# Performance work log

Measured on AMD Instinct MI355X. Metric: run time of the kernel, lower is better.

The kernel has to match this reference:

```python
import jax, jax.numpy as jnp
import numpy as np

NUM_CLASSES = 81
NEG_POS_RATIO = 3  # neg_pos init arg
POS_FRAC = 0.02    # realistic fraction of matched (positive) priors


def setup_inputs() -> dict:
    key = jax.random.key(0)
    k1, k2, k3, k4, k5 = jax.random.split(key, 5)
    B, P, C = 32, 24564, NUM_CLASSES
    loc_data = jax.random.normal(k1, (B, P, 4), jnp.float32)
    conf_data = jax.random.normal(k2, (B, P, C), jnp.float32)
    loc_targets = jax.random.normal(k3, (B, P, 4), jnp.float32)
    raw_labels = jax.random.randint(k4, (B, P), 1, C)
    is_pos = jax.random.uniform(k5, (B, P)) < POS_FRAC
    conf_targets = jnp.where(is_pos, raw_labels, 0).astype(jnp.int32)
    return {"loc_data": loc_data, "conf_data": conf_data,
            "loc_targets": loc_targets, "conf_targets": conf_targets}


def _smooth_l1(x):
    ax = jnp.abs(x)
    return jnp.where(ax < 1.0, 0.5 * x * x, ax - 0.5)


def reference(loc_data, conf_data, loc_targets, conf_targets):
    # loc_data [B,P,4], conf_data [B,P,C], conf_targets [B,P] int
    B, P, C = conf_data.shape
    pos = conf_targets > 0  # [B,P]

    # localization smooth-L1 over positive priors only (sum reduction)
    loc_loss = jnp.sum(_smooth_l1(loc_data - loc_targets) * pos[..., None].astype(loc_data.dtype))

    # per-prior CE loss: logsumexp - logit[target]
    lse = jax.nn.logsumexp(conf_data, axis=-1)  # [B,P]
    tgt_logit = jnp.take_along_axis(conf_data, conf_targets[..., None].astype(jnp.int32), axis=-1)[..., 0]
    ce = lse - tgt_logit  # [B,P]

    # hard negative mining: zero out positives, sort descending, pick pivot at 3*num_pos
    mined = jnp.where(pos, 0.0, ce)
    sorted_desc = jnp.flip(jnp.sort(mined, axis=1), axis=1)  # [B,P]
    num_pos = jnp.sum(pos, axis=1)  # [B]
    num_neg = jnp.clip(NEG_POS_RATIO * num_pos, 0, P - 1)
    pivot = jnp.take_along_axis(sorted_desc, num_neg[:, None], axis=1)  # [B,1]
    neg = mined > pivot

    sel = (pos | neg).astype(ce.dtype)
    conf_loss = jnp.sum(ce * sel)

    n_matched = jnp.maximum(jnp.sum(num_pos), 1).astype(conf_data.dtype)
    return (loc_loss + conf_loss) / n_matched
```

## Files before the change

### kernel.cpp

```cpp
#include <hip/hip_runtime.h>
#include <cmath>
#include <cstdint>

#define NB 32
#define NP 24564
#define NC 81
#define NEG_POS 3

static constexpr size_t MINED_ELEMS = (size_t)NB * NP;
static constexpr size_t MINED_BYTES = MINED_ELEMS * sizeof(float);

#define NTILES4 ((int)(MINED_ELEMS / 4))
#define MAIN_BLOCKS 2047
#define TOTAL_WAVES (MAIN_BLOCKS * 4)
#define KITERS 12


__device__ __forceinline__ float wave_reduce_sum(float v) {
#pragma unroll
  for (int off = 32; off > 0; off >>= 1) v += __shfl_down(v, off, 64);
  return v;
}

__device__ __forceinline__ float smooth_l1_4(float4 a, float4 t) {
  float acc = 0.f, d, ax;
  d = a.x - t.x; ax = fabsf(d); acc += (ax < 1.f) ? 0.5f * d * d : ax - 0.5f;
  d = a.y - t.y; ax = fabsf(d); acc += (ax < 1.f) ? 0.5f * d * d : ax - 0.5f;
  d = a.z - t.z; ax = fabsf(d); acc += (ax < 1.f) ? 0.5f * d * d : ax - 0.5f;
  d = a.w - t.w; ax = fabsf(d); acc += (ax < 1.f) ? 0.5f * d * d : ax - 0.5f;
  return acc;
}

__global__ __launch_bounds__(256, 8) void mb_main(
    const float* __restrict__ conf_data, const int* __restrict__ conf_targets,
    float* __restrict__ mined) {
  __shared__ float lds[4][332];

  const int tid  = (int)threadIdx.x;
  const int wid  = tid >> 6, lane = tid & 63;
  const int r    = lane >> 4, il = lane & 15;
  float* __restrict__ L = lds[wid];

  const int l17   = (lane < 17) ? lane : 16;
  const int ldst1 = (lane < 17) ? (256 + 4 * l17) : 328;

#define LOAD_DATA(c0, c1, t)                                            \
  do {                                                                  \
    const float4* __restrict__ _s =                                     \
        reinterpret_cast<const float4*>(conf_data) + (size_t)(t) * 81;  \
    (c0) = _s[lane];                                                    \
    (c1) = _s[64 + l17];                                                \
  } while (0)

#define STAGE(c0, c1)                                  \
  do {                                                 \
    *reinterpret_cast<float4*>(&L[4 * lane]) = (c0);   \
    *reinterpret_cast<float4*>(&L[ldst1]) = (c1);      \
  } while (0)

#define COMPUTE(t, tg)                                                  \
  do {                                                                  \
    const int tgt = (r == 0) ? (tg).x : (r == 1) ? (tg).y               \
                  : (r == 2) ? (tg).z : (tg).w;                         \
    const int rb = 81 * r;                                              \
    float e = __expf(L[rb + il]) + __expf(L[rb + il + 16]) +            \
              __expf(L[rb + il + 32]) + __expf(L[rb + il + 48]) +       \
              __expf(L[rb + il + 64]);                                  \
    if (il == 0) e += __expf(L[rb + 80]);                               \
    e += __shfl_xor(e, 1, 64);                                          \
    e += __shfl_xor(e, 2, 64);                                          \
    e += __shfl_xor(e, 4, 64);                                          \
    e += __shfl_xor(e, 8, 64);                                          \
    const float tv = L[rb + tgt];                                       \
    const float ce = __logf(e) - tv;                                    \
    const float val = (tgt > 0) ? -ce : ce;                             \
    mined[(t) * 4 + r] = val;                                           \
  } while (0)

  int tile = (int)blockIdx.x * 4 + wid;
  float4 cA0, cA1, cB0, cB1;
  int4 tg0, tg1, tgN;

  LOAD_DATA(cA0, cA1, tile);
  tg0 = *reinterpret_cast<const int4*>(conf_targets + (size_t)tile * 4);
  {
    const int tB = tile + TOTAL_WAVES;
    LOAD_DATA(cB0, cB1, tB);
    tg1 = *reinterpret_cast<const int4*>(conf_targets + (size_t)tB * 4);
  }

#pragma unroll 1
  for (int k = 0; k < KITERS; ++k) {
    STAGE(cA0, cA1);
    {
      int nt = tile + 2 * TOTAL_WAVES;
      nt = (nt < NTILES4) ? nt : tile;
      LOAD_DATA(cA0, cA1, nt);
      tgN = *reinterpret_cast<const int4*>(conf_targets + (size_t)nt * 4);
    }
    __builtin_amdgcn_sched_barrier(0);
    COMPUTE(tile, tg0);
    tg0 = tg1; tg1 = tgN;
    tile += TOTAL_WAVES;

    STAGE(cB0, cB1);
    {
      int nt = tile + 2 * TOTAL_WAVES;
      nt = (nt < NTILES4) ? nt : tile;
      LOAD_DATA(cB0, cB1, nt);
      tgN = *reinterpret_cast<const int4*>(conf_targets + (size_t)nt * 4);
    }
    __builtin_amdgcn_sched_barrier(0);
    COMPUTE(tile, tg0);
    tg0 = tg1; tg1 = tgN;
    tile += TOTAL_WAVES;
  }
#undef LOAD_DATA
#undef STAGE
#undef COMPUTE
}

__global__ __launch_bounds__(1024) void mb_select(
    const float* __restrict__ mined, const float* __restrict__ loc_data,
    const float* __restrict__ loc_targets, float* __restrict__ partial,
    int* __restrict__ num_pos) {
  const int b = blockIdx.x;
  const float* __restrict__ row = mined + (size_t)b * NP;
  const int tid = threadIdx.x;
  const int wid = tid >> 6;
  const int lane = tid & 63;

  __shared__ int hist[16][256];
  __shared__ int total[256];
  __shared__ int suffix[256];
  __shared__ unsigned s_prefix;
  __shared__ int s_k;

  for (int i = tid; i < 16 * 256; i += 1024) ((int*)hist)[i] = 0;
  __syncthreads();
  {
    int np = 0;
    float cp = 0.f, lv = 0.f;
    for (int q = tid; q < NP / 4; q += 1024) {
      const float4 v = reinterpret_cast<const float4*>(row)[q];
      const float vv[4] = {v.x, v.y, v.z, v.w};
#pragma unroll
      for (int j = 0; j < 4; ++j) {
        unsigned u = __float_as_uint(vv[j]);
        if (u >> 31) {
          np++;
          cp += -vv[j];
          const size_t flat = (size_t)b * NP + 4 * q + j;
          lv += smooth_l1_4(
              *reinterpret_cast<const float4*>(loc_data + flat * 4),
              *reinterpret_cast<const float4*>(loc_targets + flat * 4));
          u = 0u;
        }
        atomicAdd(&hist[wid][u >> 24], 1);
      }
    }
    __shared__ float rednp[16], redcp[16], redlv[16];
    float wnp = wave_reduce_sum((float)np);
    float wcp = wave_reduce_sum(cp);
    float wlv = wave_reduce_sum(lv);
    if (lane == 0) { rednp[wid] = wnp; redcp[wid] = wcp; redlv[wid] = wlv; }
    __syncthreads();
    if (tid == 0) {
      float tnp = 0.f, tcp = 0.f, tlv = 0.f;
#pragma unroll
      for (int i = 0; i < 16; ++i) { tnp += rednp[i]; tcp += redcp[i]; tlv += redlv[i]; }
      const int npi = (int)tnp;
      num_pos[b] = npi;
      partial[b * 4 + 0] = tlv;
      partial[b * 4 + 1] = tcp;
      int k = NEG_POS * npi;
      if (k > NP - 1) k = NP - 1;
      s_k = k;
      s_prefix = 0u;
    }
    __syncthreads();
  }

#define PASS_EPILOGUE(SHIFT)                                                  \
  do {                                                                        \
    if (tid < 256) {                                                          \
      int t = 0;                                                              \
      _Pragma("unroll")                                                       \
      for (int w = 0; w < 16; ++w) t += hist[w][tid];                         \
      total[tid] = t;                                                         \
    }                                                                         \
    __syncthreads();                                                          \
    if (wid == 0) {                                                           \
      const int t0_ = total[4 * lane + 0];                                    \
      const int t1_ = total[4 * lane + 1];                                    \
      const int t2_ = total[4 * lane + 2];                                    \
      const int t3_ = total[4 * lane + 3];                                    \
      const int s3 = t3_;                                                     \
      const int s2 = t2_ + s3;                                                \
      const int s1 = t1_ + s2;                                                \
      const int s0 = t0_ + s1;                                                \
      int acc_ = s0;                                                          \
      _Pragma("unroll")                                                       \
      for (int off = 1; off < 64; off <<= 1) {                                \
        const int o = __shfl_down(acc_, off, 64);                             \
        if (lane + off < 64) acc_ += o;                                       \
      }                                                                       \
      const int excl = acc_ - s0;                                             \
      suffix[4 * lane + 0] = s0 + excl;                                       \
      suffix[4 * lane + 1] = s1 + excl;                                       \
      suffix[4 * lane + 2] = s2 + excl;                                       \
      suffix[4 * lane + 3] = s3 + excl;                                       \
    }                                                                         \
    __syncthreads();                                                          \
    if (tid < 256) {                                                          \
      const int kcur = s_k;                                                   \
      const int cs = suffix[tid] - total[tid];                                \
      if (kcur >= cs && kcur < cs + total[tid]) {                             \
        s_prefix |= ((unsigned)tid << (SHIFT));                               \
        s_k = kcur - cs;                                                      \
      }                                                                       \
    }                                                                         \
    __syncthreads();                                                          \
  } while (0)

  PASS_EPILOGUE(24);

  for (int shift = 16; shift >= 0; shift -= 8) {
    for (int i = tid; i < 16 * 256; i += 1024) ((int*)hist)[i] = 0;
    __syncthreads();
    const unsigned mask = 0xFFFFFFFFu << (shift + 8);
    const unsigned pfx = s_prefix;

    for (int q = tid; q < NP / 4; q += 1024) {
      const float4 v = reinterpret_cast<const float4*>(row)[q];
      unsigned u;
      u = __float_as_uint(v.x); u = (u >> 31) ? 0u : u; if ((u & mask) == pfx) atomicAdd(&hist[wid][(u >> shift) & 255], 1);
      u = __float_as_uint(v.y); u = (u >> 31) ? 0u : u; if ((u & mask) == pfx) atomicAdd(&hist[wid][(u >> shift) & 255], 1);
      u = __float_as_uint(v.z); u = (u >> 31) ? 0u : u; if ((u & mask) == pfx) atomicAdd(&hist[wid][(u >> shift) & 255], 1);
      u = __float_as_uint(v.w); u = (u >> 31) ? 0u : u; if ((u & mask) == pfx) atomicAdd(&hist[wid][(u >> shift) & 255], 1);
    }
    __syncthreads();

    if (shift == 16) PASS_EPILOGUE(16);
    else if (shift == 8) PASS_EPILOGUE(8);
    else PASS_EPILOGUE(0);
  }
#undef PASS_EPILOGUE

  const unsigned vbits = s_prefix;
  float sum = 0.f;
  for (int q = tid; q < NP / 4; q += 1024) {
    const float4 v = reinterpret_cast<const float4*>(row)[q];
    unsigned u;
    u = __float_as_uint(v.x); u = (u >> 31) ? 0u : u; if (u > vbits) sum += v.x;
    u = __float_as_uint(v.y); u = (u >> 31) ? 0u : u; if (u > vbits) sum += v.y;
    u = __float_as_uint(v.z); u = (u >> 31) ? 0u : u; if (u > vbits) sum += v.z;
    u = __float_as_uint(v.w); u = (u >> 31) ? 0u : u; if (u > vbits) sum += v.w;
  }

  __shared__ float wsum[16];
  float w = wave_reduce_sum(sum);
  if (lane == 0) wsum[wid] = w;
  __syncthreads();
  if (tid == 0) {
    float t = 0.f;
#pragma unroll
    for (int i = 0; i < 16; ++i) t += wsum[i];
    partial[b * 4 + 2] = t;
  }
}

__global__ void mb_finalize(const float* __restrict__ partial,
                            const int* __restrict__ num_pos,
                            float* __restrict__ out) {
  if (threadIdx.x == 0) {
    double s = 0.0;
    int tot = 0;
#pragma unroll
    for (int i = 0; i < NB; ++i) {
      s += (double)partial[i * 4 + 0] + (double)partial[i * 4 + 1] +
           (double)partial[i * 4 + 2];
      tot += num_pos[i];
    }
    const double n = (double)(tot > 0 ? tot : 1);
    out[0] = (float)(s / n);
  }
}

extern "C" void kernel_launch(void* const* d_in, const int* in_sizes, int n_in,
                              void* d_out, int out_size, void* d_ws, size_t ws_size,
                              hipStream_t stream) {
  const float* loc_data     = (const float*)d_in[0];
  const float* conf_data    = (const float*)d_in[1];
  const float* loc_targets  = (const float*)d_in[2];
  const int*   conf_targets = (const int*)d_in[3];
  float* out = (float*)d_out;

  float* mined   = (float*)d_ws;
  float* partial = (float*)((char*)d_ws + MINED_BYTES);
  int*   num_pos = (int*)((char*)d_ws + MINED_BYTES + 512);

  mb_main<<<MAIN_BLOCKS, 256, 0, stream>>>(conf_data, conf_targets, mined);

  mb_select<<<NB, 1024, 0, stream>>>(mined, loc_data, loc_targets, partial, num_pos);

  mb_finalize<<<1, 64, 0, stream>>>(partial, num_pos, out);
}
```

Measured before the change: 85.41 us.

## Process eight priors per wave tile instead of four in CE kernel

Each wave now loads and stages 8 priors (648 floats) per tile with three float4 loads per lane. Eight lanes per prior compute the logsumexp, which shortens the shuffle reduction by one step, and the loop count is halved. Target loads go through readfirstlane so they become scalar loads. This gives more bytes in flight per wave and fewer iterations, at the cost of doubled LDS per wave and more registers, which may reduce occupancy.

```diff
diff --git a/kernel.cpp b/kernel.cpp
--- a/kernel.cpp
+++ b/kernel.cpp
@@ -10,10 +10,10 @@
 static constexpr size_t MINED_ELEMS = (size_t)NB * NP;
 static constexpr size_t MINED_BYTES = MINED_ELEMS * sizeof(float);
 
-#define NTILES4 ((int)(MINED_ELEMS / 4))
+#define NTILES8 ((int)(MINED_ELEMS / 8))
 #define MAIN_BLOCKS 2047
 #define TOTAL_WAVES (MAIN_BLOCKS * 4)
-#define KITERS 12
+#define KITERS 6
 
 
 __device__ __forceinline__ float wave_reduce_sum(float v) {
@@ -34,88 +34,102 @@
 __global__ __launch_bounds__(256, 8) void mb_main(
     const float* __restrict__ conf_data, const int* __restrict__ conf_targets,
     float* __restrict__ mined) {
-  __shared__ float lds[4][332];
+  __shared__ float lds[4][656];
 
   const int tid  = (int)threadIdx.x;
   const int wid  = tid >> 6, lane = tid & 63;
-  const int r    = lane >> 4, il = lane & 15;
+  const int r    = lane >> 3, il = lane & 7;
   float* __restrict__ L = lds[wid];
 
-  const int l17   = (lane < 17) ? lane : 16;
-  const int ldst1 = (lane < 17) ? (256 + 4 * l17) : 328;
-
-#define LOAD_DATA(c0, c1, t)                                            \
+  const int src3  = 128 + ((lane < 34) ? lane : 33);
+  const int ldst3 = (lane < 34) ? (4 * (128 + lane)) : 648;
+
+#define LOAD_DATA(c0, c1, c2, t)                                        \
   do {                                                                  \
     const float4* __restrict__ _s =                                     \
-        reinterpret_cast<const float4*>(conf_data) + (size_t)(t) * 81;  \
+        reinterpret_cast<const float4*>(conf_data) + (size_t)(t) * 162; \
     (c0) = _s[lane];                                                    \
-    (c1) = _s[64 + l17];                                                \
-  } while (0)
-
-#define STAGE(c0, c1)                                  \
-  do {                                                 \
-    *reinterpret_cast<float4*>(&L[4 * lane]) = (c0);   \
-    *reinterpret_cast<float4*>(&L[ldst1]) = (c1);      \
-  } while (0)
-
-#define COMPUTE(t, tg)                                                  \
+    (c1) = _s[64 + lane];                                               \
+    (c2) = _s[src3];                                                    \
+  } while (0)
+
+#define LOAD_TG(ta, tb, t)                                                   \
+  do {                                                                       \
+    const int _ut = __builtin_amdgcn_readfirstlane(t);                       \
+    (ta) = *reinterpret_cast<const int4*>(conf_targets + (size_t)_ut * 8);   \
+    (tb) = *reinterpret_cast<const int4*>(conf_targets + (size_t)_ut * 8 + 4); \
+  } while (0)
+
+#define STAGE(c0, c1, c2)                                   \
+  do {                                                      \
+    *reinterpret_cast<float4*>(&L[4 * lane]) = (c0);        \
+    *reinterpret_cast<float4*>(&L[4 * (64 + lane)]) = (c1); \
+    *reinterpret_cast<float4*>(&L[ldst3]) = (c2);           \
+  } while (0)
+
+#define COMPUTE(t, ta, tb)                                              \
   do {                                                                  \
-    const int tgt = (r == 0) ? (tg).x : (r == 1) ? (tg).y               \
-                  : (r == 2) ? (tg).z : (tg).w;                         \
+    const int tgt = (r < 4)                                             \
+        ? ((r == 0) ? (ta).x : (r == 1) ? (ta).y                        \
+           : (r == 2) ? (ta).z : (ta).w)                                \
+        : ((r == 4) ? (tb).x : (r == 5) ? (tb).y                        \
+           : (r == 6) ? (tb).z : (tb).w);                               \
     const int rb = 81 * r;                                              \
-    float e = __expf(L[rb + il]) + __expf(L[rb + il + 16]) +            \
-              __expf(L[rb + il + 32]) + __expf(L[rb + il + 48]) +       \
-              __expf(L[rb + il + 64]);                                  \
+    float e = __expf(L[rb + il])      + __expf(L[rb + il + 8]) +        \
+              __expf(L[rb + il + 16]) + __expf(L[rb + il + 24]) +       \
+              __expf(L[rb + il + 32]) + __expf(L[rb + il + 40]) +       \
+              __expf(L[rb + il + 48]) + __expf(L[rb + il + 56]) +       \
+              __expf(L[rb + il + 64]) + __expf(L[rb + il + 72]);        \
     if (il == 0) e += __expf(L[rb + 80]);                               \
     e += __shfl_xor(e, 1, 64);                                          \
     e += __shfl_xor(e, 2, 64);                                          \
     e += __shfl_xor(e, 4, 64);                                          \
-    e += __shfl_xor(e, 8, 64);                                          \
     const float tv = L[rb + tgt];                                       \
     const float ce = __logf(e) - tv;                                    \
     const float val = (tgt > 0) ? -ce : ce;                             \
-    mined[(t) * 4 + r] = val;                                           \
+    if (il == 0) mined[(t) * 8 + r] = val;                              \
   } while (0)
 
   int tile = (int)blockIdx.x * 4 + wid;
-  float4 cA0, cA1, cB0, cB1;
-  int4 tg0, tg1, tgN;
-
-  LOAD_DATA(cA0, cA1, tile);
-  tg0 = *reinterpret_cast<const int4*>(conf_targets + (size_t)tile * 4);
+  float4 cA0, cA1, cA2, cB0, cB1, cB2;
+  int4 taA, tbA, taB, tbB, taN, tbN;
+
+  LOAD_DATA(cA0, cA1, cA2, tile);
+  LOAD_TG(taA, tbA, tile);
   {
     const int tB = tile + TOTAL_WAVES;
-    LOAD_DATA(cB0, cB1, tB);
-    tg1 = *reinterpret_cast<const int4*>(conf_targets + (size_t)tB * 4);
+    LOAD_DATA(cB0, cB1, cB2, tB);
+    LOAD_TG(taB, tbB, tB);
   }
 
 #pragma unroll 1
   for (int k = 0; k < KITERS; ++k) {
-    STAGE(cA0, cA1);
+    STAGE(cA0, cA1, cA2);
     {
       int nt = tile + 2 * TOTAL_WAVES;
-      nt = (nt < NTILES4) ? nt : tile;
-      LOAD_DATA(cA0, cA1, nt);
-      tgN = *reinterpret_cast<const int4*>(conf_targets + (size_t)nt * 4);
+      nt = (nt < NTILES8) ? nt : tile;
+      LOAD_DATA(cA0, cA1, cA2, nt);
+      LOAD_TG(taN, tbN, nt);
     }
     __builtin_amdgcn_sched_barrier(0);
-    COMPUTE(tile, tg0);
-    tg0 = tg1; tg1 = tgN;
+    COMPUTE(tile, taA, tbA);
+    taA = taB; tbA = tbB; taB = taN; tbB = tbN;
     tile += TOTAL_WAVES;
 
-    STAGE(cB0, cB1);
+    STAGE(cB0, cB1, cB2);
     {
       int nt = tile + 2 * TOTAL_WAVES;
-      nt = (nt < NTILES4) ? nt : tile;
-      LOAD_DATA(cB0, cB1, nt);
-      tgN = *reinterpret_cast<const int4*>(conf_targets + (size_t)nt * 4);
+      nt = (nt < NTILES8) ? nt : tile;
+      LOAD_DATA(cB0, cB1, cB2, nt);
+      LOAD_TG(taN, tbN, nt);
     }
     __builtin_amdgcn_sched_barrier(0);
-    COMPUTE(tile, tg0);
-    tg0 = tg1; tg1 = tgN;
+    COMPUTE(tile, taA, tbA);
+    taA = taB; tbA = tbB; taB = taN; tbB = tbN;
     tile += TOTAL_WAVES;
   }
 #undef LOAD_DATA
+#undef LOAD_TG
 #undef STAGE
 #undef COMPUTE
 }
```

New measurement: 85.82 us. About the same (+0.5%).
